# Kernel tuning notes

Hardware: AMD Instinct MI355X
Metric: run time of the kernel (lower is better)

Reference implementation:

```python
import jax, jax.numpy as jnp
import numpy as np

N = 100000   # nodes
E = 1600000  # edges
D = 128      # input_dim == hidden_dim
L = 3        # n_layers
P = 7        # n_properties
B = 64       # graphs in batch
BN_EPS = 1e-5
NEG_SLOPE = 0.2


def setup_inputs() -> dict:
    key = jax.random.key(0)
    ks = jax.random.split(key, 18)
    s = 1.0 / np.sqrt(D)
    sp = 1.0 / np.sqrt(P)
    return {
        "x": jax.random.normal(ks[0], (N, D), jnp.float32),
        "edge_index": jax.random.randint(ks[1], (2, E), 0, N, dtype=jnp.int64),
        "batch": jnp.sort(jax.random.randint(ks[2], (N,), 0, B, dtype=jnp.int64)),
        "graph_stats": jax.random.normal(ks[3], (B, P), jnp.float32),
        # GIN MLP params (stacked over layers; input_dim == hidden_dim == D)
        "W1s": jax.random.normal(ks[4], (L, D, D), jnp.float32) * s,
        "b1s": jnp.zeros((L, D), jnp.float32),
        "gammas": jnp.ones((L, D), jnp.float32),
        "betas": jnp.zeros((L, D), jnp.float32),
        "bn_means": jax.random.normal(ks[5], (L, D), jnp.float32) * 0.1,
        "bn_vars": jax.random.uniform(ks[6], (L, D), jnp.float32) + 0.5,
        "W2s": jax.random.normal(ks[7], (L, D, D), jnp.float32) * s,
        "b2s": jnp.zeros((L, D), jnp.float32),
        # stat conditioning transforms
        "statWs": jax.random.normal(ks[8], (L, P, D), jnp.float32) * sp,
        "statBs": jnp.zeros((L, D), jnp.float32),
        # fc_out
        "fcW": jax.random.normal(ks[9], (D, D), jnp.float32) * s,
        "fcB": jnp.zeros((D,), jnp.float32),
    }


def reference(x, edge_index, batch, graph_stats,
              W1s, b1s, gammas, betas, bn_means, bn_vars, W2s, b2s,
              statWs, statBs, fcW, fcB):
    # per-node graph stats (nan -> -100, then broadcast by graph id)
    node_stats = jnp.nan_to_num(graph_stats, nan=-100.0)[batch]  # [N, P]
    src, dst = edge_index[0], edge_index[1]
    h = x
    for i in range(L):
        # GIN aggregation (eps = 0): (1+eps)*h_i + sum_{j->i} h_j
        agg = jax.ops.segment_sum(h[src], dst, num_segments=N)  # [N, D]
        m = h + agg
        # MLP: Linear -> LeakyReLU(0.2) -> BatchNorm1d (eval) -> Linear -> LeakyReLU(0.2)
        m = jax.nn.leaky_relu(m @ W1s[i] + b1s[i], NEG_SLOPE)
        m = (m - bn_means[i]) * (gammas[i] / jnp.sqrt(bn_vars[i] + BN_EPS)) + betas[i]
        m = jax.nn.leaky_relu(m @ W2s[i] + b2s[i], NEG_SLOPE)
        # stats conditioning add (dropout is identity in eval mode)
        h = m + node_stats @ statWs[i] + statBs[i]
    return h @ fcW + fcB  # [N, D]
```

## Files before the change

kernel.cpp:

```cpp
#include <hip/hip_runtime.h>
#include <math.h>

#define N_NODES 100000
#define N_EDGES 1600000
#define D 128
#define L_LAYERS 3
#define P_STATS 7
#define B_GRAPHS 64
#define BN_EPS 1e-5f
#define NEG_SLOPE 0.2f

#define NB 196
#define BCAP 10240
#define EPB 6400

typedef __attribute__((ext_vector_type(8))) short bf16x8;
typedef __attribute__((ext_vector_type(4))) float f32x4;

static __device__ __forceinline__ short f2bf(float f) {
    union { float f; unsigned u; } v;
    v.f = f;
    unsigned r = v.u + 0x7fffu + ((v.u >> 16) & 1u);
    return (short)(r >> 16);
}

static __device__ __forceinline__ float bf2f(short s) {
    union { unsigned u; float f; } v;
    v.u = ((unsigned)(unsigned short)s) << 16;
    return v.f;
}

__global__ __launch_bounds__(256) void setup_kernel(const float* __restrict__ W1s,
                                                    const float* __restrict__ W2s,
                                                    const float* __restrict__ fcW,
                                                    short* __restrict__ wt,
                                                    const float* __restrict__ gs,
                                                    const float* __restrict__ statWs,
                                                    const float* __restrict__ statBs,
                                                    float* __restrict__ gproj,
                                                    int* __restrict__ bucket_cnt) {
    const int bid = blockIdx.x;
    const int tid = threadIdx.x;
    if (bid < 448) {
        int mid = bid >> 6;
        int chunk = bid & 63;
        const float* src = (mid < 3) ? (W1s + mid * D * D)
                                     : ((mid < 6) ? (W2s + (mid - 3) * D * D) : fcW);
        short* dstm = wt + mid * D * D;
        int i = chunk * 256 + tid;
        int k = i >> 7, n = i & 127;
        dstm[n * D + k] = f2bf(src[i]);
    } else if (bid < 448 + 96) {
        int p = (bid - 448) * 2 + (tid >> 7);
        int j = tid & 127;
        int b = p & 63;
        int l = p >> 6;
        float acc = statBs[l * D + j];
#pragma unroll
        for (int q = 0; q < P_STATS; ++q) {
            float g = gs[b * P_STATS + q];
            if (g != g) g = -100.0f;
            acc += g * statWs[(l * P_STATS + q) * D + j];
        }
        gproj[(l * B_GRAPHS + b) * D + j] = acc;
    } else {
        if (tid < NB) bucket_cnt[tid] = 0;
    }
}

__global__ __launch_bounds__(256) void bucketA_kernel(const int* __restrict__ src,
                                                      const int* __restrict__ dst,
                                                      int* __restrict__ bucket_cnt,
                                                      int* __restrict__ bucketbuf) {
    __shared__ int hist[NB], base[NB], loc[NB];
    const int tid = threadIdx.x;
    const int e0 = blockIdx.x * EPB;
    for (int i = tid; i < NB; i += 256) { hist[i] = 0; loc[i] = 0; }
    __syncthreads();
    for (int i = tid; i < EPB; i += 256) {
        int d = dst[e0 + i];
        atomicAdd(&hist[d >> 9], 1);
    }
    __syncthreads();
    for (int i = tid; i < NB; i += 256)
        base[i] = hist[i] ? atomicAdd(&bucket_cnt[i], hist[i]) : 0;
    __syncthreads();
    for (int i = tid; i < EPB; i += 256) {
        int s = src[e0 + i];
        int d = dst[e0 + i];
        int b = d >> 9;
        int off = atomicAdd(&loc[b], 1);
        int idx = base[b] + off;
        if (idx < BCAP) bucketbuf[(size_t)b * BCAP + idx] = (s << 9) | (d & 511);
    }
}

__global__ __launch_bounds__(256) void bucketB_kernel(const int* __restrict__ bucket_cnt,
                                                      const int* __restrict__ bucketbuf,
                                                      int* __restrict__ start,
                                                      int* __restrict__ csr_src) {
    __shared__ int hist[512];
    __shared__ int incl[512];
    __shared__ int cursor[512];
    __shared__ int red[256];
    __shared__ int sbase_sh;
    const int b = blockIdx.x;
    const int tid = threadIdx.x;
    const int cnt_b = min(bucket_cnt[b], BCAP);

    int partial = 0;
    for (int i = tid; i < b; i += 256) partial += min(bucket_cnt[i], BCAP);
    red[tid] = partial;
    __syncthreads();
    for (int off = 128; off > 0; off >>= 1) {
        if (tid < off) red[tid] += red[tid + off];
        __syncthreads();
    }
    if (tid == 0) sbase_sh = red[0];

    hist[tid] = 0;
    hist[tid + 256] = 0;
    __syncthreads();
    const int* bb = bucketbuf + (size_t)b * BCAP;
    for (int i = tid; i < cnt_b; i += 256) atomicAdd(&hist[bb[i] & 511], 1);
    __syncthreads();
    incl[tid] = hist[tid];
    incl[tid + 256] = hist[tid + 256];
    __syncthreads();
    for (int off = 1; off < 512; off <<= 1) {
        int i1 = tid + 256;
        int v0 = (tid >= off) ? incl[tid - off] : 0;
        int v1 = (i1 >= off) ? incl[i1 - off] : 0;
        __syncthreads();
        incl[tid] += v0;
        incl[i1] += v1;
        __syncthreads();
    }
    const int sbase = sbase_sh;
    int excl0 = incl[tid] - hist[tid];
    int excl1 = incl[tid + 256] - hist[tid + 256];
    cursor[tid] = excl0;
    cursor[tid + 256] = excl1;
    const int nbase = b << 9;
    if (nbase + tid < N_NODES) start[nbase + tid] = sbase + excl0;
    if (nbase + tid + 256 < N_NODES) start[nbase + tid + 256] = sbase + excl1;
    if (b == NB - 1 && tid == 0) start[N_NODES] = sbase + incl[511];
    __syncthreads();
    for (int i = tid; i < cnt_b; i += 256) {
        int e = bb[i];
        int pos = atomicAdd(&cursor[e & 511], 1);
        csr_src[sbase + pos] = e >> 9;
    }
}

__global__ __launch_bounds__(256) void agg_ep_kernel(const short* __restrict__ g,
                                                     const int* __restrict__ start,
                                                     const int* __restrict__ csr_src,
                                                     const float* __restrict__ b1,
                                                     const float* __restrict__ gamma,
                                                     const float* __restrict__ beta,
                                                     const float* __restrict__ mean,
                                                     const float* __restrict__ var,
                                                     short* __restrict__ z) {
    int node = blockIdx.x * 16 + (threadIdx.x >> 4);
    int c8 = threadIdx.x & 15;
    const bf16x8* g8 = (const bf16x8*)g;

    bf16x8 own = g8[node * 16 + c8];
    float acc[8];
#pragma unroll
    for (int i = 0; i < 8; ++i) acc[i] = bf2f(own[i]);

    int s = start[node];
    int e = start[node + 1];
    int k = s;
    for (; k + 4 <= e; k += 4) {
        int sn0 = csr_src[k];
        int sn1 = csr_src[k + 1];
        int sn2 = csr_src[k + 2];
        int sn3 = csr_src[k + 3];
        bf16x8 v0 = g8[sn0 * 16 + c8];
        bf16x8 v1 = g8[sn1 * 16 + c8];
        bf16x8 v2 = g8[sn2 * 16 + c8];
        bf16x8 v3 = g8[sn3 * 16 + c8];
#pragma unroll
        for (int i = 0; i < 8; ++i) acc[i] += bf2f(v0[i]);
#pragma unroll
        for (int i = 0; i < 8; ++i) acc[i] += bf2f(v1[i]);
#pragma unroll
        for (int i = 0; i < 8; ++i) acc[i] += bf2f(v2[i]);
#pragma unroll
        for (int i = 0; i < 8; ++i) acc[i] += bf2f(v3[i]);
    }
    for (; k < e; ++k) {
        int sn0 = csr_src[k];
        bf16x8 v0 = g8[sn0 * 16 + c8];
#pragma unroll
        for (int i = 0; i < 8; ++i) acc[i] += bf2f(v0[i]);
    }

    const int f0 = c8 * 8;
    float4 bb0 = *(const float4*)&b1[f0];
    float4 bb1 = *(const float4*)&b1[f0 + 4];
    float4 gm0 = *(const float4*)&gamma[f0];
    float4 gm1 = *(const float4*)&gamma[f0 + 4];
    float4 bt0 = *(const float4*)&beta[f0];
    float4 bt1 = *(const float4*)&beta[f0 + 4];
    float4 mn0 = *(const float4*)&mean[f0];
    float4 mn1 = *(const float4*)&mean[f0 + 4];
    float4 vr0 = *(const float4*)&var[f0];
    float4 vr1 = *(const float4*)&var[f0 + 4];
    float bbv[8] = {bb0.x, bb0.y, bb0.z, bb0.w, bb1.x, bb1.y, bb1.z, bb1.w};
    float gmv[8] = {gm0.x, gm0.y, gm0.z, gm0.w, gm1.x, gm1.y, gm1.z, gm1.w};
    float btv[8] = {bt0.x, bt0.y, bt0.z, bt0.w, bt1.x, bt1.y, bt1.z, bt1.w};
    float mnv[8] = {mn0.x, mn0.y, mn0.z, mn0.w, mn1.x, mn1.y, mn1.z, mn1.w};
    float vrv[8] = {vr0.x, vr0.y, vr0.z, vr0.w, vr1.x, vr1.y, vr1.z, vr1.w};

    short pk[8];
#pragma unroll
    for (int i = 0; i < 8; ++i) {
        float t = acc[i] + bbv[i];
        t = (t > 0.f) ? t : NEG_SLOPE * t;
        float sc = gmv[i] * rsqrtf(vrv[i] + BN_EPS);
        t = t * sc + (btv[i] - mnv[i] * sc);
        pk[i] = f2bf(t);
    }
    *(bf16x8*)&z[node * D + f0] = *(bf16x8*)pk;
}

__global__ __launch_bounds__(256, 4) void initgemm_kernel(const float* __restrict__ x,
                                                          const short* __restrict__ Wt,
                                                          short* __restrict__ g_out) {
    __shared__ short sy[64 * 128];
    const int tid = threadIdx.x;
    const int wid = tid >> 6;
    const int lane = tid & 63;
    const int lr = lane & 15;
    const int lk = lane >> 4;

    const int nlBase = (wid >> 1) * 32;
    const int nodeBase = blockIdx.x * 64 + nlBase;
    const int featBase = (wid & 1) * 64;

    int nIdx[2];
#pragma unroll
    for (int mt = 0; mt < 2; ++mt) {
        int n = nodeBase + mt * 16 + lr;
        nIdx[mt] = (n < N_NODES) ? n : (N_NODES - 1);
    }

    f32x4 acc[4][2];
#pragma unroll
    for (int ft = 0; ft < 4; ++ft)
#pragma unroll
        for (int mt = 0; mt < 2; ++mt)
            acc[ft][mt] = (f32x4)(0.0f);

#pragma unroll
    for (int kt = 0; kt < 4; ++kt) {
        bf16x8 wfk[4];
#pragma unroll
        for (int ft = 0; ft < 4; ++ft)
            wfk[ft] = *(const bf16x8*)&Wt[(featBase + ft * 16 + lr) * D + kt * 32 + lk * 8];
        bf16x8 mf[2];
#pragma unroll
        for (int mt = 0; mt < 2; ++mt) {
            const float4* xp = (const float4*)&x[nIdx[mt] * D + kt * 32 + lk * 8];
            float4 a = xp[0], b = xp[1];
            short q[8];
            q[0] = f2bf(a.x); q[1] = f2bf(a.y); q[2] = f2bf(a.z); q[3] = f2bf(a.w);
            q[4] = f2bf(b.x); q[5] = f2bf(b.y); q[6] = f2bf(b.z); q[7] = f2bf(b.w);
            mf[mt] = *(bf16x8*)q;
        }
#pragma unroll
        for (int ft = 0; ft < 4; ++ft)
#pragma unroll
            for (int mt = 0; mt < 2; ++mt)
                acc[ft][mt] = __builtin_amdgcn_mfma_f32_16x16x32_bf16(wfk[ft], mf[mt],
                                                                      acc[ft][mt], 0, 0, 0);
    }

#pragma unroll
    for (int ft = 0; ft < 4; ++ft) {
        int f0 = featBase + ft * 16 + lk * 4;
#pragma unroll
        for (int mt = 0; mt < 2; ++mt) {
            int nl = nlBase + mt * 16 + lr;
            short4 pk;
#pragma unroll
            for (int r = 0; r < 4; ++r) ((short*)&pk)[r] = f2bf(acc[ft][mt][r]);
            int byteoff = nl * 256 + f0 * 2;
            byteoff ^= (nl & 7) << 4;
            *(short4*)((char*)sy + byteoff) = pk;
        }
    }
    __syncthreads();
#pragma unroll
    for (int it = 0; it < 4; ++it) {
        int c = tid + it * 256;
        int nl = c >> 4;
        int c8 = c & 15;
        int node = blockIdx.x * 64 + nl;
        if (node < N_NODES) {
            int byteoff = nl * 256 + c8 * 16;
            byteoff ^= (nl & 7) << 4;
            bf16x8 v = *(const bf16x8*)((char*)sy + byteoff);
            *(bf16x8*)&g_out[node * D + c8 * 8] = v;
        }
    }
}

template <bool FINAL>
__global__ __launch_bounds__(256, 4) void mlp2_kernel(
    const short* __restrict__ z,
    const short* __restrict__ W2t,
    const float* __restrict__ b2,
    const float* __restrict__ gproj, const int* __restrict__ batch,
    const short* __restrict__ Wnt,
    const float* __restrict__ fcb,
    float* __restrict__ outf, short* __restrict__ g_out) {
    __shared__ short sy[64 * 128];
    __shared__ float sB2[128], sFC[128];

    const int tid = threadIdx.x;
    const int wid = tid >> 6;
    const int lane = tid & 63;
    const int lr = lane & 15;
    const int lk = lane >> 4;

    if (tid < 128) {
        sB2[tid] = b2[tid];
        if (FINAL) sFC[tid] = fcb[tid];
    }
    __syncthreads();

    const int nlBase = (wid >> 1) * 32;
    const int nodeBase = blockIdx.x * 64 + nlBase;
    const int featBase = (wid & 1) * 64;

    int nIdx[2];
#pragma unroll
    for (int mt = 0; mt < 2; ++mt) {
        int n = nodeBase + mt * 16 + lr;
        nIdx[mt] = (n < N_NODES) ? n : (N_NODES - 1);
    }

    f32x4 acc[4][2];
#pragma unroll
    for (int ft = 0; ft < 4; ++ft)
#pragma unroll
        for (int mt = 0; mt < 2; ++mt)
            acc[ft][mt] = (f32x4)(0.0f);

#pragma unroll
    for (int kt = 0; kt < 4; ++kt) {
        bf16x8 wfk[4];
#pragma unroll
        for (int ft = 0; ft < 4; ++ft)
            wfk[ft] = *(const bf16x8*)&W2t[(featBase + ft * 16 + lr) * D + kt * 32 + lk * 8];
        bf16x8 zf[2];
#pragma unroll
        for (int mt = 0; mt < 2; ++mt)
            zf[mt] = *(const bf16x8*)&z[nIdx[mt] * D + kt * 32 + lk * 8];
#pragma unroll
        for (int ft = 0; ft < 4; ++ft)
#pragma unroll
            for (int mt = 0; mt < 2; ++mt)
                acc[ft][mt] = __builtin_amdgcn_mfma_f32_16x16x32_bf16(wfk[ft], zf[mt],
                                                                      acc[ft][mt], 0, 0, 0);
    }

#pragma unroll
    for (int ft = 0; ft < 4; ++ft) {
        int f0 = featBase + ft * 16 + lk * 4;
#pragma unroll
        for (int mt = 0; mt < 2; ++mt) {
            int nl = nlBase + mt * 16 + lr;
            int bid = batch[nIdx[mt]];
            const float4 gp = *(const float4*)&gproj[bid * D + f0];
            short4 pk;
            float v0 = acc[ft][mt][0] + sB2[f0 + 0]; v0 = (v0 > 0.f) ? v0 : NEG_SLOPE * v0; v0 += gp.x;
            float v1 = acc[ft][mt][1] + sB2[f0 + 1]; v1 = (v1 > 0.f) ? v1 : NEG_SLOPE * v1; v1 += gp.y;
            float v2 = acc[ft][mt][2] + sB2[f0 + 2]; v2 = (v2 > 0.f) ? v2 : NEG_SLOPE * v2; v2 += gp.z;
            float v3 = acc[ft][mt][3] + sB2[f0 + 3]; v3 = (v3 > 0.f) ? v3 : NEG_SLOPE * v3; v3 += gp.w;
            pk.x = f2bf(v0); pk.y = f2bf(v1); pk.z = f2bf(v2); pk.w = f2bf(v3);
            int byteoff = nl * 256 + f0 * 2;
            byteoff ^= (nl & 7) << 4;
            *(short4*)((char*)sy + byteoff) = pk;
        }
    }
    __syncthreads();

#pragma unroll
    for (int ft = 0; ft < 4; ++ft)
#pragma unroll
        for (int mt = 0; mt < 2; ++mt)
            acc[ft][mt] = (f32x4)(0.0f);

#pragma unroll
    for (int kt = 0; kt < 4; ++kt) {
        bf16x8 wfk[4];
#pragma unroll
        for (int ft = 0; ft < 4; ++ft)
            wfk[ft] = *(const bf16x8*)&Wnt[(featBase + ft * 16 + lr) * D + kt * 32 + lk * 8];
        bf16x8 hf[2];
#pragma unroll
        for (int mt = 0; mt < 2; ++mt) {
            int nl = nlBase + mt * 16 + lr;
            int byteoff = nl * 256 + kt * 64 + lk * 16;
            byteoff ^= (nl & 7) << 4;
            hf[mt] = *(const bf16x8*)((char*)sy + byteoff);
        }
#pragma unroll
        for (int ft = 0; ft < 4; ++ft)
#pragma unroll
            for (int mt = 0; mt < 2; ++mt)
                acc[ft][mt] = __builtin_amdgcn_mfma_f32_16x16x32_bf16(wfk[ft], hf[mt],
                                                                      acc[ft][mt], 0, 0, 0);
    }

    if (FINAL) {
#pragma unroll
        for (int mt = 0; mt < 2; ++mt) {
            int node = nodeBase + mt * 16 + lr;
            if (node >= N_NODES) continue;
#pragma unroll
            for (int ft = 0; ft < 4; ++ft) {
                int f0 = featBase + ft * 16 + lk * 4;
                float4 o;
                o.x = acc[ft][mt][0] + sFC[f0 + 0];
                o.y = acc[ft][mt][1] + sFC[f0 + 1];
                o.z = acc[ft][mt][2] + sFC[f0 + 2];
                o.w = acc[ft][mt][3] + sFC[f0 + 3];
                *(float4*)&outf[node * D + f0] = o;
            }
        }
        return;
    }

    __syncthreads();
#pragma unroll
    for (int ft = 0; ft < 4; ++ft) {
        int f0 = featBase + ft * 16 + lk * 4;
#pragma unroll
        for (int mt = 0; mt < 2; ++mt) {
            int nl = nlBase + mt * 16 + lr;
            short4 pk;
#pragma unroll
            for (int r = 0; r < 4; ++r) ((short*)&pk)[r] = f2bf(acc[ft][mt][r]);
            int byteoff = nl * 256 + f0 * 2;
            byteoff ^= (nl & 7) << 4;
            *(short4*)((char*)sy + byteoff) = pk;
        }
    }
    __syncthreads();
#pragma unroll
    for (int it = 0; it < 4; ++it) {
        int c = tid + it * 256;
        int nl = c >> 4;
        int c8 = c & 15;
        int node = blockIdx.x * 64 + nl;
        if (node < N_NODES) {
            int byteoff = nl * 256 + c8 * 16;
            byteoff ^= (nl & 7) << 4;
            bf16x8 v = *(const bf16x8*)((char*)sy + byteoff);
            *(bf16x8*)&g_out[node * D + c8 * 8] = v;
        }
    }
}


extern "C" void kernel_launch(void* const* d_in, const int* in_sizes, int n_in,
                              void* d_out, int out_size, void* d_ws, size_t ws_size,
                              hipStream_t stream) {
    const float* x = (const float*)d_in[0];
    const int* ei = (const int*)d_in[1];
    const int* src = ei;
    const int* dst = ei + N_EDGES;
    const int* batch = (const int*)d_in[2];
    const float* gs = (const float*)d_in[3];
    const float* W1s = (const float*)d_in[4];
    const float* b1s = (const float*)d_in[5];
    const float* gammas = (const float*)d_in[6];
    const float* betas = (const float*)d_in[7];
    const float* means = (const float*)d_in[8];
    const float* vars = (const float*)d_in[9];
    const float* W2s = (const float*)d_in[10];
    const float* b2s = (const float*)d_in[11];
    const float* statWs = (const float*)d_in[12];
    const float* statBs = (const float*)d_in[13];
    const float* fcW = (const float*)d_in[14];
    const float* fcB = (const float*)d_in[15];
    float* out = (float*)d_out;

    char* ws = (char*)d_ws;
    auto alloc = [&](size_t bytes) {
        char* p = ws;
        ws += (bytes + 255) / 256 * 256;
        return p;
    };
    int* start = (int*)alloc((N_NODES + 1) * sizeof(int));
    int* csr_src = (int*)alloc(N_EDGES * sizeof(int));
    int* bucket_cnt = (int*)alloc(NB * sizeof(int));
    int* bucketbuf = (int*)alloc((size_t)NB * BCAP * sizeof(int));
    float* gproj = (float*)alloc((size_t)L_LAYERS * B_GRAPHS * D * sizeof(float));
    short* wt = (short*)alloc((size_t)7 * D * D * sizeof(short));
    short* g_buf = (short*)alloc((size_t)N_NODES * D * sizeof(short));
    short* z_buf = (short*)alloc((size_t)N_NODES * D * sizeof(short));

    setup_kernel<<<545, 256, 0, stream>>>(W1s, W2s, fcW, wt, gs, statWs, statBs, gproj,
                                          bucket_cnt);
    bucketA_kernel<<<N_EDGES / EPB, 256, 0, stream>>>(src, dst, bucket_cnt, bucketbuf);
    bucketB_kernel<<<NB, 256, 0, stream>>>(bucket_cnt, bucketbuf, start, csr_src);

    const int agg_blocks = N_NODES / 16;
    const int mlp_blocks = (N_NODES + 63) / 64;

    initgemm_kernel<<<mlp_blocks, 256, 0, stream>>>(x, wt + 0 * D * D, g_buf);

    agg_ep_kernel<<<agg_blocks, 256, 0, stream>>>(g_buf, start, csr_src, b1s + 0 * D,
                                                  gammas + 0 * D, betas + 0 * D, means + 0 * D,
                                                  vars + 0 * D, z_buf);
    mlp2_kernel<false><<<mlp_blocks, 256, 0, stream>>>(
        z_buf, wt + 3 * D * D, b2s + 0 * D, gproj + 0 * B_GRAPHS * D, batch,
        wt + 1 * D * D, nullptr, nullptr, g_buf);
    agg_ep_kernel<<<agg_blocks, 256, 0, stream>>>(g_buf, start, csr_src, b1s + 1 * D,
                                                  gammas + 1 * D, betas + 1 * D, means + 1 * D,
                                                  vars + 1 * D, z_buf);
    mlp2_kernel<false><<<mlp_blocks, 256, 0, stream>>>(
        z_buf, wt + 4 * D * D, b2s + 1 * D, gproj + 1 * B_GRAPHS * D, batch,
        wt + 2 * D * D, nullptr, nullptr, g_buf);
    agg_ep_kernel<<<agg_blocks, 256, 0, stream>>>(g_buf, start, csr_src, b1s + 2 * D,
                                                  gammas + 2 * D, betas + 2 * D, means + 2 * D,
                                                  vars + 2 * D, z_buf);
    mlp2_kernel<true><<<mlp_blocks, 256, 0, stream>>>(
        z_buf, wt + 5 * D * D, b2s + 2 * D, gproj + 2 * B_GRAPHS * D, batch,
        wt + 6 * D * D, fcB, out, nullptr);
}
```

Baseline: 385.4 us.

## Remap node blocks per XCD and deepen gather unroll with nontemporal index loads

Block indices are remapped so that each of the 8 XCDs handles a contiguous range of node blocks in the aggregation, init GEMM and MLP kernels. The goal is that a node's z/g rows are produced and consumed on the same XCD, which keeps them in that XCD's L2. The grid is padded to 1568 blocks, so out-of-range nodes get an early return or bounds guard. The aggregation loop also gains an 8-way unrolled gather for more memory-level parallelism, and CSR index loads become nontemporal so they do not pollute the cache. Risks are higher register pressure from the deeper unroll and the assumption that blocks are dispatched round-robin across XCDs.

```diff
diff --git a/kernel.cpp b/kernel.cpp
--- a/kernel.cpp
+++ b/kernel.cpp
@@ -13,6 +13,10 @@
 #define NB 196
 #define BCAP 10240
 #define EPB 6400
+
+#define NXCD 8
+#define NBK 1568
+#define NBK_PER_XCD (NBK / NXCD)
 
 typedef __attribute__((ext_vector_type(8))) short bf16x8;
 typedef __attribute__((ext_vector_type(4))) float f32x4;
@@ -162,7 +166,11 @@
                                                      const float* __restrict__ mean,
                                                      const float* __restrict__ var,
                                                      short* __restrict__ z) {
-    int node = blockIdx.x * 16 + (threadIdx.x >> 4);
+    const int xcd = blockIdx.x & 7;
+    const int t = blockIdx.x >> 3;
+    const int nb = xcd * NBK_PER_XCD + (t >> 2);
+    int node = nb * 64 + (t & 3) * 16 + (threadIdx.x >> 4);
+    if (node >= N_NODES) return;
     int c8 = threadIdx.x & 15;
     const bf16x8* g8 = (const bf16x8*)g;
 
@@ -174,11 +182,23 @@
     int s = start[node];
     int e = start[node + 1];
     int k = s;
+    for (; k + 8 <= e; k += 8) {
+        int sn[8];
+#pragma unroll
+        for (int j = 0; j < 8; ++j) sn[j] = __builtin_nontemporal_load(&csr_src[k + j]);
+        bf16x8 v[8];
+#pragma unroll
+        for (int j = 0; j < 8; ++j) v[j] = g8[sn[j] * 16 + c8];
+#pragma unroll
+        for (int j = 0; j < 8; ++j)
+#pragma unroll
+            for (int i = 0; i < 8; ++i) acc[i] += bf2f(v[j][i]);
+    }
     for (; k + 4 <= e; k += 4) {
-        int sn0 = csr_src[k];
-        int sn1 = csr_src[k + 1];
-        int sn2 = csr_src[k + 2];
-        int sn3 = csr_src[k + 3];
+        int sn0 = __builtin_nontemporal_load(&csr_src[k]);
+        int sn1 = __builtin_nontemporal_load(&csr_src[k + 1]);
+        int sn2 = __builtin_nontemporal_load(&csr_src[k + 2]);
+        int sn3 = __builtin_nontemporal_load(&csr_src[k + 3]);
         bf16x8 v0 = g8[sn0 * 16 + c8];
         bf16x8 v1 = g8[sn1 * 16 + c8];
         bf16x8 v2 = g8[sn2 * 16 + c8];
@@ -193,7 +213,7 @@
         for (int i = 0; i < 8; ++i) acc[i] += bf2f(v3[i]);
     }
     for (; k < e; ++k) {
-        int sn0 = csr_src[k];
+        int sn0 = __builtin_nontemporal_load(&csr_src[k]);
         bf16x8 v0 = g8[sn0 * 16 + c8];
 #pragma unroll
         for (int i = 0; i < 8; ++i) acc[i] += bf2f(v0[i]);
@@ -219,11 +239,11 @@
     short pk[8];
 #pragma unroll
     for (int i = 0; i < 8; ++i) {
-        float t = acc[i] + bbv[i];
-        t = (t > 0.f) ? t : NEG_SLOPE * t;
+        float t2 = acc[i] + bbv[i];
+        t2 = (t2 > 0.f) ? t2 : NEG_SLOPE * t2;
         float sc = gmv[i] * rsqrtf(vrv[i] + BN_EPS);
-        t = t * sc + (btv[i] - mnv[i] * sc);
-        pk[i] = f2bf(t);
+        t2 = t2 * sc + (btv[i] - mnv[i] * sc);
+        pk[i] = f2bf(t2);
     }
     *(bf16x8*)&z[node * D + f0] = *(bf16x8*)pk;
 }
@@ -238,8 +258,12 @@
     const int lr = lane & 15;
     const int lk = lane >> 4;
 
+    const int xcd = blockIdx.x & 7;
+    const int nb = xcd * NBK_PER_XCD + (blockIdx.x >> 3);
+    const int blockNode = nb * 64;
+
     const int nlBase = (wid >> 1) * 32;
-    const int nodeBase = blockIdx.x * 64 + nlBase;
+    const int nodeBase = blockNode + nlBase;
     const int featBase = (wid & 1) * 64;
 
     int nIdx[2];
@@ -300,7 +324,7 @@
         int c = tid + it * 256;
         int nl = c >> 4;
         int c8 = c & 15;
-        int node = blockIdx.x * 64 + nl;
+        int node = blockNode + nl;
         if (node < N_NODES) {
             int byteoff = nl * 256 + c8 * 16;
             byteoff ^= (nl & 7) << 4;
@@ -334,8 +358,12 @@
     }
     __syncthreads();
 
+    const int xcd = blockIdx.x & 7;
+    const int nb = xcd * NBK_PER_XCD + (blockIdx.x >> 3);
+    const int blockNode = nb * 64;
+
     const int nlBase = (wid >> 1) * 32;
-    const int nodeBase = blockIdx.x * 64 + nlBase;
+    const int nodeBase = blockNode + nlBase;
     const int featBase = (wid & 1) * 64;
 
     int nIdx[2];
@@ -459,7 +487,7 @@
         int c = tid + it * 256;
         int nl = c >> 4;
         int c8 = c & 15;
-        int node = blockIdx.x * 64 + nl;
+        int node = blockNode + nl;
         if (node < N_NODES) {
             int byteoff = nl * 256 + c8 * 16;
             byteoff ^= (nl & 7) << 4;
@@ -513,8 +541,8 @@
     bucketA_kernel<<<N_EDGES / EPB, 256, 0, stream>>>(src, dst, bucket_cnt, bucketbuf);
     bucketB_kernel<<<NB, 256, 0, stream>>>(bucket_cnt, bucketbuf, start, csr_src);
 
-    const int agg_blocks = N_NODES / 16;
-    const int mlp_blocks = (N_NODES + 63) / 64;
+    const int agg_blocks = NBK * 4;
+    const int mlp_blocks = NBK;
 
     initgemm_kernel<<<mlp_blocks, 256, 0, stream>>>(x, wt + 0 * D * D, g_buf);
 
```

New measurement: 400.8 us. +4.0%, slower.
